# Kernel tuning notes

Measured on AMD Instinct MI355X. Metric: run time of the kernel, lower is better.

Reference implementation:

```python
import jax, jax.numpy as jnp
import numpy as np
from jax import lax

N, M, T, V, C_IN, C_OUT, KT, PAD = 16, 2, 300, 25, 64, 64, 9, 4
BN_EPS = 1e-5

# NTU-RGB+D 25-joint skeleton edges (0-indexed), symmetric, plus self-loops
_NTU_EDGES = [(0,1),(1,20),(2,20),(3,2),(4,20),(5,4),(6,5),(7,6),(8,20),(9,8),
              (10,9),(11,10),(12,0),(13,12),(14,13),(15,14),(16,0),(17,16),
              (18,17),(19,18),(21,22),(22,7),(23,24),(24,11)]

def _build_adj():
    A = np.zeros((V, V), dtype=np.float32)
    for i, j in _NTU_EDGES:
        A[i, j] = 1.0
        A[j, i] = 1.0
    A += np.eye(V, dtype=np.float32)  # self-loops (DGL GCN preprocessing)
    return jnp.asarray(A)


def setup_inputs() -> dict:
    key = jax.random.key(0)
    ks = jax.random.split(key, 8)
    stdv = 1.0 / np.sqrt(C_OUT)
    # conv_init: normal(0, sqrt(2/(out_channels*prod(kernel))))
    conv_std = np.sqrt(2.0 / (C_OUT * KT * 1))
    return {
        "h": jax.random.normal(ks[0], (N * M * T * V, C_IN), dtype=jnp.float32),
        "adj": _build_adj(),
        "gcn_w": jax.random.uniform(ks[1], (C_IN, C_OUT), minval=-stdv, maxval=stdv, dtype=jnp.float32),
        "gcn_b": jax.random.uniform(ks[2], (C_OUT,), minval=-stdv, maxval=stdv, dtype=jnp.float32),
        "conv_w": conv_std * jax.random.normal(ks[3], (C_OUT, C_OUT, KT, 1), dtype=jnp.float32),
        "conv_b": jnp.zeros((C_OUT,), dtype=jnp.float32),
        "bn_gamma": jnp.ones((C_OUT,), dtype=jnp.float32),
        "bn_beta": jnp.zeros((C_OUT,), dtype=jnp.float32),
        "bn_mean": 0.1 * jax.random.normal(ks[4], (C_OUT,), dtype=jnp.float32),
        "bn_var": jax.random.uniform(ks[5], (C_OUT,), minval=0.5, maxval=1.5, dtype=jnp.float32),
    }


def reference(h, adj, gcn_w, gcn_b, conv_w, conv_b, bn_gamma, bn_beta, bn_mean, bn_var):
    # ---- GCNLayer (dropout is identity at eval) ----
    # symmetric norm = deg^{-1/2}, identical across the N*M*T copies of the skeleton
    norm = adj.sum(axis=1) ** -0.5                      # (V,)
    x = h @ gcn_w                                        # (N*M*T*V, C_OUT)
    x = x.reshape(-1, V, C_OUT) * norm[:, None]          # pre-norm scale
    x = jnp.einsum('vu,buc->bvc', adj, x)                # copy_src + sum aggregation
    x = x * norm[:, None] + gcn_b                        # post-norm scale + bias
    x = jax.nn.relu(x)

    # ---- TemporalConvNetwork ----
    v = x.reshape(N, M, T, V, C_OUT)
    v = v.transpose(0, 1, 4, 2, 3).reshape(N * M, C_OUT, T, V)   # (NM, C, T, V)
    v = lax.conv_general_dilated(v, conv_w, window_strides=(1, 1),
                                 padding=[(PAD, PAD), (0, 0)],
                                 dimension_numbers=('NCHW', 'OIHW', 'NCHW'))
    v = v + conv_b[None, :, None, None]
    inv_std = bn_gamma / jnp.sqrt(bn_var + BN_EPS)       # eval-mode BatchNorm2d
    v = (v - bn_mean[None, :, None, None]) * inv_std[None, :, None, None] + bn_beta[None, :, None, None]
    v = jax.nn.relu(v)
    v = v.reshape(N, M, C_OUT, T, V).transpose(0, 1, 3, 4, 2)    # (N, M, T, V, C)

    # ---- residual (downt is None since in_feats == out_feats and stride == 1) ----
    return v + h.reshape(N, M, T, V, C_IN)
```

## Files before the change

### kernel.cpp

```cpp
#include <hip/hip_runtime.h>
#include <hip/hip_bf16.h>


typedef __bf16 bf16x8 __attribute__((ext_vector_type(8)));
typedef __bf16 bf16x4 __attribute__((ext_vector_type(4)));
typedef float  f32x4  __attribute__((ext_vector_type(4)));

#define Y_OFF   0
#define WC2_OFF 30720000
#define WGT_OFF 30793728
#define A2P_OFF 30801920
#define SC_OFF  30803968
#define SH_OFF  30804224

__global__ __launch_bounds__(256) void prep_kernel(
    const float* __restrict__ adj, const float* __restrict__ gcn_w,
    const float* __restrict__ conv_w, const float* __restrict__ conv_b,
    const float* __restrict__ bn_g, const float* __restrict__ bn_b,
    const float* __restrict__ bn_m, const float* __restrict__ bn_v,
    __bf16* __restrict__ wc2, __bf16* __restrict__ wgt,
    __bf16* __restrict__ a2p, float* __restrict__ scale, float* __restrict__ shift) {
  int tid = threadIdx.x;
  for (int e = blockIdx.x * 256 + tid; e < 36864; e += gridDim.x * 256) {
    int j = e & 7, t1 = e >> 3, c = t1 & 63, g = t1 >> 6;
    int kap = g * 8 + j, kt = kap >> 6, ci = kap & 63;
    wc2[e] = (__bf16)conv_w[(c * 64 + ci) * 9 + kt];
  }
  if (blockIdx.x == 0) {
    for (int e = tid; e < 4096; e += 256) {
      int c = e >> 6, k = e & 63;
      wgt[e] = (__bf16)gcn_w[k * 64 + c];
    }
  } else if (blockIdx.x == 1) {
    for (int e = tid; e < 1024; e += 256) {
      int v = e >> 5, u = e & 31;
      float val = 0.f;
      if (v < 25 && u < 25) {
        float dv = 0.f, du = 0.f;
        for (int t = 0; t < 25; ++t) { dv += adj[v * 25 + t]; du += adj[u * 25 + t]; }
        val = rsqrtf(dv) * adj[v * 25 + u] * rsqrtf(du);
      }
      a2p[e] = (__bf16)val;
    }
  } else if (blockIdx.x == 2) {
    if (tid < 64) {
      float sc = bn_g[tid] * rsqrtf(bn_v[tid] + 1e-5f);
      scale[tid] = sc;
      shift[tid] = (conv_b[tid] - bn_m[tid]) * sc + bn_b[tid];
    }
  }
}

__global__ __launch_bounds__(256) void gcn_kernel(
    const float* __restrict__ h, const __bf16* __restrict__ wgt_g,
    const __bf16* __restrict__ a2p_g, const float* __restrict__ gcn_b,
    __bf16* __restrict__ y) {
  __shared__ __align__(16) __bf16 wgT[64 * 72];
  __shared__ __align__(16) __bf16 a2p[32 * 40];
  __shared__ __align__(16) __bf16 hb[4][32 * 72];
  __shared__ __align__(16) __bf16 x1t[4][64 * 40];
  int tid = threadIdx.x, w = tid >> 6, lane = tid & 63;
  int l15 = lane & 15, quad = lane >> 4;

  {
    for (int e = tid; e < 512; e += 256) {
      uint4 val = ((const uint4*)wgt_g)[e];
      *(uint4*)&wgT[(e >> 3) * 72 + (e & 7) * 8] = val;
    }
    if (tid < 128) {
      uint4 val = ((const uint4*)a2p_g)[tid];
      *(uint4*)&a2p[(tid >> 2) * 40 + (tid & 3) * 8] = val;
    }
  }
  __syncthreads();

  int skel = blockIdx.x * 4 + w;
  int nm = skel / 300, tloc = skel - nm * 300;
  for (int e = lane; e < 7 * 72; e += 64) hb[w][25 * 72 + e] = (__bf16)0.f;
  for (int it = 0; it < 7; ++it) {
    int u = it * 4 + quad;
    if (u < 25) {
      float4 hv = *(const float4*)&h[(skel * 25 + u) * 64 + l15 * 4];
      bf16x4 b; b[0] = (__bf16)hv.x; b[1] = (__bf16)hv.y; b[2] = (__bf16)hv.z; b[3] = (__bf16)hv.w;
      *(bf16x4*)&hb[w][u * 72 + l15 * 4] = b;
    }
  }
  for (int mt = 0; mt < 4; ++mt)
    for (int nt = 0; nt < 2; ++nt) {
      f32x4 acc = {0.f, 0.f, 0.f, 0.f};
      for (int kk = 0; kk < 2; ++kk) {
        bf16x8 a = *(const bf16x8*)&wgT[(mt * 16 + l15) * 72 + kk * 32 + quad * 8];
        bf16x8 b = *(const bf16x8*)&hb[w][(nt * 16 + l15) * 72 + kk * 32 + quad * 8];
        acc = __builtin_amdgcn_mfma_f32_16x16x32_bf16(a, b, acc, 0, 0, 0);
      }
      int u = nt * 16 + l15, c0 = mt * 16 + quad * 4;
      for (int r = 0; r < 4; ++r) x1t[w][(c0 + r) * 40 + u] = (__bf16)acc[r];
    }
  for (int mt = 0; mt < 4; ++mt)
    for (int nt = 0; nt < 2; ++nt) {
      f32x4 acc = {0.f, 0.f, 0.f, 0.f};
      bf16x8 a = *(const bf16x8*)&x1t[w][(mt * 16 + l15) * 40 + quad * 8];
      bf16x8 b = *(const bf16x8*)&a2p[(nt * 16 + l15) * 40 + quad * 8];
      acc = __builtin_amdgcn_mfma_f32_16x16x32_bf16(a, b, acc, 0, 0, 0);
      int v = nt * 16 + l15, c0 = mt * 16 + quad * 4;
      if (v < 25) {
        float4 bias = *(const float4*)&gcn_b[c0];
        hb[w][v * 80 + c0 + 0] = (__bf16)fmaxf(acc[0] + bias.x, 0.f);
        hb[w][v * 80 + c0 + 1] = (__bf16)fmaxf(acc[1] + bias.y, 0.f);
        hb[w][v * 80 + c0 + 2] = (__bf16)fmaxf(acc[2] + bias.z, 0.f);
        hb[w][v * 80 + c0 + 3] = (__bf16)fmaxf(acc[3] + bias.w, 0.f);
      }
    }
  for (int e = lane; e < 200; e += 64) {
    int v = e >> 3, ch = e & 7;
    uint4 val = *(const uint4*)&hb[w][v * 80 + ch * 8];
    *(uint4*)&y[((nm * 25 + v) * 300 + tloc) * 64 + ch * 8] = val;
  }
}

__global__ __launch_bounds__(256) void conv_kernel(
    const __bf16* __restrict__ y, const __bf16* __restrict__ wc2,
    const float* __restrict__ scale, const float* __restrict__ shift,
    const float* __restrict__ h, float* __restrict__ out) {
  __shared__ __align__(16) __bf16 ylds[4 * 72 * 64];
  int tid = threadIdx.x, w = tid >> 6, lane = tid & 63;
  int l15 = lane & 15, quad = lane >> 4;
  int gid = blockIdx.x * 4 + w;
  int ti = gid % 5, r1 = gid / 5;
  int vv = r1 % 25, nm = r1 / 25;
  int t0 = (ti < 4) ? ti * 64 : 236;

  __bf16* my = &ylds[w * 4608];
  {
    const __bf16* ybase = &y[((nm * 25 + vv) * 300) * 64];
    uint4 stg[9];
    for (int it = 0; it < 9; ++it) {
      int idx = it * 64 + lane, r = idx >> 3, ch = idx & 7;
      int tg = t0 - 4 + r;
      uint4 val = {0u, 0u, 0u, 0u};
      if (tg >= 0 && tg < 300) val = *(const uint4*)&ybase[tg * 64 + ch * 8];
      stg[it] = val;
    }
    for (int it = 0; it < 9; ++it) {
      int idx = it * 64 + lane, r = idx >> 3, ch = idx & 7;
      *(uint4*)&my[r * 64 + ((ch ^ (r & 7)) * 8)] = stg[it];
    }
  }

  f32x4 acc[4][4];
  for (int m = 0; m < 4; ++m) for (int n = 0; n < 4; ++n) acc[m][n] = (f32x4){0.f, 0.f, 0.f, 0.f};

  bf16x8 a0[4], a1[4];
#define LOADA(dst, kk_) { const __bf16* wb = wc2 + (((kk_) * 4 + quad) * 64) * 8; \
    for (int m = 0; m < 4; ++m) dst[m] = *(const bf16x8*)&wb[(m * 16 + l15) * 8]; }
#define COMPUTE(kk_, areg) { int kt = (kk_) >> 1, chb = ((kk_) & 1) * 4 + quad; \
    for (int n = 0; n < 4; ++n) { \
      int row = n * 16 + l15 + kt; \
      bf16x8 b = *(const bf16x8*)&my[row * 64 + ((chb ^ (row & 7)) * 8)]; \
      for (int m = 0; m < 4; ++m) \
        acc[m][n] = __builtin_amdgcn_mfma_f32_16x16x32_bf16(areg[m], b, acc[m][n], 0, 0, 0); \
    } }
  LOADA(a0, 0)
  for (int kk = 0; kk < 18; kk += 2) {
    LOADA(a1, kk + 1)
    COMPUTE(kk, a0)
    if (kk + 2 < 18) LOADA(a0, kk + 2)
    COMPUTE(kk + 1, a1)
  }
#undef LOADA
#undef COMPUTE

  for (int n = 0; n < 4; ++n) {
    int tt = t0 + n * 16 + l15;
    for (int m = 0; m < 4; ++m) {
      int c0 = m * 16 + quad * 4;
      int idx = ((nm * 300 + tt) * 25 + vv) * 64 + c0;
      float4 sc = *(const float4*)&scale[c0];
      float4 sh = *(const float4*)&shift[c0];
      float4 hr = *(const float4*)&h[idx];
      float4 o;
      o.x = fmaxf(acc[m][n][0] * sc.x + sh.x, 0.f) + hr.x;
      o.y = fmaxf(acc[m][n][1] * sc.y + sh.y, 0.f) + hr.y;
      o.z = fmaxf(acc[m][n][2] * sc.z + sh.z, 0.f) + hr.z;
      o.w = fmaxf(acc[m][n][3] * sc.w + sh.w, 0.f) + hr.w;
      *(float4*)&out[idx] = o;
    }
  }
}

extern "C" void kernel_launch(void* const* d_in, const int* in_sizes, int n_in,
                              void* d_out, int out_size, void* d_ws, size_t ws_size,
                              hipStream_t stream) {
  const float* h      = (const float*)d_in[0];
  const float* adj    = (const float*)d_in[1];
  const float* gcn_w  = (const float*)d_in[2];
  const float* gcn_b  = (const float*)d_in[3];
  const float* conv_w = (const float*)d_in[4];
  const float* conv_b = (const float*)d_in[5];
  const float* bn_g   = (const float*)d_in[6];
  const float* bn_b   = (const float*)d_in[7];
  const float* bn_m   = (const float*)d_in[8];
  const float* bn_v   = (const float*)d_in[9];
  float* out = (float*)d_out;
  char* ws = (char*)d_ws;

  __bf16* y_ws   = (__bf16*)(ws + Y_OFF);
  __bf16* wc2    = (__bf16*)(ws + WC2_OFF);
  __bf16* wgt    = (__bf16*)(ws + WGT_OFF);
  __bf16* a2p    = (__bf16*)(ws + A2P_OFF);
  float*  scale  = (float*)(ws + SC_OFF);
  float*  shift  = (float*)(ws + SH_OFF);

  prep_kernel<<<64, 256, 0, stream>>>(adj, gcn_w, conv_w, conv_b, bn_g, bn_b, bn_m, bn_v,
                                      wc2, wgt, a2p, scale, shift);
  gcn_kernel<<<2400, 256, 0, stream>>>(h, wgt, a2p, gcn_b, y_ws);
  conv_kernel<<<1000, 256, 0, stream>>>(y_ws, wc2, scale, shift, h, out);
}
```

Before: 172.6 us.

## Keep GCN weights in registers, swizzle LDS, and split conv into single-wave blocks

The GCN kernel now loads the weight and adjacency MFMA fragments straight from global memory into registers. This removes the shared-memory staging and the block-wide barrier, and it shrinks LDS by using XOR-swizzled 64-wide rows instead of padded ones. The conv kernel is relaunched as 4000 one-wave blocks instead of 1000 four-wave blocks, so each block needs less LDS and can be scheduled independently. The cost is higher register pressure in the GCN kernel, since every wave keeps its own weight fragments, and more global or L2 loads of the weights.

```diff
diff --git a/kernel.cpp b/kernel.cpp
--- a/kernel.cpp
+++ b/kernel.cpp
@@ -51,86 +51,82 @@
   }
 }
 
-__global__ __launch_bounds__(256) void gcn_kernel(
+__global__ __launch_bounds__(256, 4) void gcn_kernel(
     const float* __restrict__ h, const __bf16* __restrict__ wgt_g,
     const __bf16* __restrict__ a2p_g, const float* __restrict__ gcn_b,
     __bf16* __restrict__ y) {
-  __shared__ __align__(16) __bf16 wgT[64 * 72];
-  __shared__ __align__(16) __bf16 a2p[32 * 40];
-  __shared__ __align__(16) __bf16 hb[4][32 * 72];
-  __shared__ __align__(16) __bf16 x1t[4][64 * 40];
+  __shared__ __align__(16) __bf16 hb[4][2048];
+  __shared__ __align__(16) __bf16 x1t[4][2048];
   int tid = threadIdx.x, w = tid >> 6, lane = tid & 63;
   int l15 = lane & 15, quad = lane >> 4;
-
-  {
-    for (int e = tid; e < 512; e += 256) {
-      uint4 val = ((const uint4*)wgt_g)[e];
-      *(uint4*)&wgT[(e >> 3) * 72 + (e & 7) * 8] = val;
-    }
-    if (tid < 128) {
-      uint4 val = ((const uint4*)a2p_g)[tid];
-      *(uint4*)&a2p[(tid >> 2) * 40 + (tid & 3) * 8] = val;
-    }
-  }
-  __syncthreads();
-
   int skel = blockIdx.x * 4 + w;
   int nm = skel / 300, tloc = skel - nm * 300;
-  for (int e = lane; e < 7 * 72; e += 64) hb[w][25 * 72 + e] = (__bf16)0.f;
+
+  bf16x8 awg[4][2];
+  for (int mt = 0; mt < 4; ++mt)
+    for (int kk = 0; kk < 2; ++kk)
+      awg[mt][kk] = *(const bf16x8*)&wgt_g[(mt * 16 + l15) * 64 + kk * 32 + quad * 8];
+  bf16x8 ba[2];
+  for (int nt = 0; nt < 2; ++nt)
+    ba[nt] = *(const bf16x8*)&a2p_g[(nt * 16 + l15) * 32 + quad * 8];
+
+  if (lane < 56) *(uint4*)&hb[w][1600 + lane * 8] = (uint4){0u, 0u, 0u, 0u};
   for (int it = 0; it < 7; ++it) {
     int u = it * 4 + quad;
     if (u < 25) {
       float4 hv = *(const float4*)&h[(skel * 25 + u) * 64 + l15 * 4];
-      bf16x4 b; b[0] = (__bf16)hv.x; b[1] = (__bf16)hv.y; b[2] = (__bf16)hv.z; b[3] = (__bf16)hv.w;
-      *(bf16x4*)&hb[w][u * 72 + l15 * 4] = b;
+      bf16x4 b4; b4[0] = (__bf16)hv.x; b4[1] = (__bf16)hv.y; b4[2] = (__bf16)hv.z; b4[3] = (__bf16)hv.w;
+      int ch = l15 >> 1;
+      *(bf16x4*)&hb[w][u * 64 + (((ch ^ (u & 7)) * 8) | ((l15 & 1) * 4))] = b4;
     }
   }
   for (int mt = 0; mt < 4; ++mt)
     for (int nt = 0; nt < 2; ++nt) {
       f32x4 acc = {0.f, 0.f, 0.f, 0.f};
+      int u = nt * 16 + l15;
       for (int kk = 0; kk < 2; ++kk) {
-        bf16x8 a = *(const bf16x8*)&wgT[(mt * 16 + l15) * 72 + kk * 32 + quad * 8];
-        bf16x8 b = *(const bf16x8*)&hb[w][(nt * 16 + l15) * 72 + kk * 32 + quad * 8];
-        acc = __builtin_amdgcn_mfma_f32_16x16x32_bf16(a, b, acc, 0, 0, 0);
+        bf16x8 b = *(const bf16x8*)&hb[w][u * 64 + (((kk * 4 + quad) ^ (u & 7)) * 8)];
+        acc = __builtin_amdgcn_mfma_f32_16x16x32_bf16(awg[mt][kk], b, acc, 0, 0, 0);
       }
-      int u = nt * 16 + l15, c0 = mt * 16 + quad * 4;
-      for (int r = 0; r < 4; ++r) x1t[w][(c0 + r) * 40 + u] = (__bf16)acc[r];
+      int c0 = mt * 16 + quad * 4;
+      for (int r = 0; r < 4; ++r) x1t[w][(c0 + r) * 32 + u] = (__bf16)acc[r];
     }
   for (int mt = 0; mt < 4; ++mt)
     for (int nt = 0; nt < 2; ++nt) {
       f32x4 acc = {0.f, 0.f, 0.f, 0.f};
-      bf16x8 a = *(const bf16x8*)&x1t[w][(mt * 16 + l15) * 40 + quad * 8];
-      bf16x8 b = *(const bf16x8*)&a2p[(nt * 16 + l15) * 40 + quad * 8];
-      acc = __builtin_amdgcn_mfma_f32_16x16x32_bf16(a, b, acc, 0, 0, 0);
+      bf16x8 a = *(const bf16x8*)&x1t[w][(mt * 16 + l15) * 32 + quad * 8];
+      acc = __builtin_amdgcn_mfma_f32_16x16x32_bf16(a, ba[nt], acc, 0, 0, 0);
       int v = nt * 16 + l15, c0 = mt * 16 + quad * 4;
       if (v < 25) {
         float4 bias = *(const float4*)&gcn_b[c0];
-        hb[w][v * 80 + c0 + 0] = (__bf16)fmaxf(acc[0] + bias.x, 0.f);
-        hb[w][v * 80 + c0 + 1] = (__bf16)fmaxf(acc[1] + bias.y, 0.f);
-        hb[w][v * 80 + c0 + 2] = (__bf16)fmaxf(acc[2] + bias.z, 0.f);
-        hb[w][v * 80 + c0 + 3] = (__bf16)fmaxf(acc[3] + bias.w, 0.f);
+        bf16x4 o;
+        o[0] = (__bf16)fmaxf(acc[0] + bias.x, 0.f);
+        o[1] = (__bf16)fmaxf(acc[1] + bias.y, 0.f);
+        o[2] = (__bf16)fmaxf(acc[2] + bias.z, 0.f);
+        o[3] = (__bf16)fmaxf(acc[3] + bias.w, 0.f);
+        int ch = (c0 >> 3) ^ (v & 7);
+        *(bf16x4*)&hb[w][v * 64 + ((ch * 8) | (c0 & 7))] = o;
       }
     }
   for (int e = lane; e < 200; e += 64) {
     int v = e >> 3, ch = e & 7;
-    uint4 val = *(const uint4*)&hb[w][v * 80 + ch * 8];
+    uint4 val = *(const uint4*)&hb[w][v * 64 + ((ch ^ (v & 7)) * 8)];
     *(uint4*)&y[((nm * 25 + v) * 300 + tloc) * 64 + ch * 8] = val;
   }
 }
 
-__global__ __launch_bounds__(256) void conv_kernel(
+__global__ __launch_bounds__(64, 4) void conv_kernel(
     const __bf16* __restrict__ y, const __bf16* __restrict__ wc2,
     const float* __restrict__ scale, const float* __restrict__ shift,
     const float* __restrict__ h, float* __restrict__ out) {
-  __shared__ __align__(16) __bf16 ylds[4 * 72 * 64];
-  int tid = threadIdx.x, w = tid >> 6, lane = tid & 63;
+  __shared__ __align__(16) __bf16 my[72 * 64];
+  int lane = threadIdx.x;
   int l15 = lane & 15, quad = lane >> 4;
-  int gid = blockIdx.x * 4 + w;
+  int gid = blockIdx.x;
   int ti = gid % 5, r1 = gid / 5;
   int vv = r1 % 25, nm = r1 / 25;
   int t0 = (ti < 4) ? ti * 64 : 236;
 
-  __bf16* my = &ylds[w * 4608];
   {
     const __bf16* ybase = &y[((nm * 25 + vv) * 300) * 64];
     uint4 stg[9];
@@ -214,5 +210,5 @@
   prep_kernel<<<64, 256, 0, stream>>>(adj, gcn_w, conv_w, conv_b, bn_g, bn_b, bn_m, bn_v,
                                       wc2, wgt, a2p, scale, shift);
   gcn_kernel<<<2400, 256, 0, stream>>>(h, wgt, a2p, gcn_b, y_ws);
-  conv_kernel<<<1000, 256, 0, stream>>>(y_ws, wc2, scale, shift, h, out);
-}
+  conv_kernel<<<4000, 64, 0, stream>>>(y_ws, wc2, scale, shift, h, out);
+}
```

Result: no change. 174.2 us (+0.9%).
